# Optimization experiments

Hardware: AMD Instinct MI355X
Metric: run time of the kernel (lower is better)

## Reference

```python
import jax, jax.numpy as jnp
import numpy as np

NLAT, NLON = 64, 64
CIN = 512
HEADS = 8


def _cc_weights(n):
    # Clenshaw-Curtis quadrature weights on [-1, 1] for nodes cos(k*pi/(n-1)),
    # as used by torch-harmonics for the 'equiangular' grid. Weights sum to 2.
    N = n - 1
    theta = np.pi * np.arange(n) / N
    m = N // 2
    j = np.arange(1, m + 1)
    b = np.where(2 * j == N, 1.0, 2.0)
    S = (b / (4.0 * j ** 2 - 1.0))[None, :] * np.cos(2.0 * j[None, :] * theta[:, None])
    w = 1.0 - S.sum(axis=1)
    c = np.full(n, 2.0)
    c[0] = 1.0
    c[-1] = 1.0
    return c * w / N


def _log_quad_weights(nlat, nlon):
    # _precompute_latitudes flips nodes/weights; then 2*pi*w/nlon tiled over lon.
    w = _cc_weights(nlat)[::-1].copy()
    qw = 2.0 * np.pi * w / nlon                       # (nlat,)
    qw = np.tile(qw[:, None], (1, nlon)).reshape(-1)  # (nlat*nlon,)
    return jnp.asarray(np.log(qw), dtype=jnp.float32)


def setup_inputs() -> dict:
    key = jax.random.key(0)
    ks = jax.random.split(key, 5)
    s_qkv = float(np.sqrt(3.0 / CIN))   # scale for q/k/v 1x1-conv weights
    s_proj = float(np.sqrt(3.0 / CIN))  # out_channels == CIN
    u = lambda k, sh, s: jax.random.uniform(k, sh, jnp.float32, -s, s)
    return dict(
        query=jax.random.normal(ks[0], (1, CIN, NLAT, NLON), jnp.float32),
        q_w=u(ks[1], (CIN, CIN), s_qkv), q_b=jnp.zeros((CIN,), jnp.float32),
        k_w=u(ks[2], (CIN, CIN), s_qkv), k_b=jnp.zeros((CIN,), jnp.float32),
        v_w=u(ks[3], (CIN, CIN), s_qkv), v_b=jnp.zeros((CIN,), jnp.float32),
        p_w=u(ks[4], (CIN, CIN), s_proj), p_b=jnp.zeros((CIN,), jnp.float32),
        log_quad_weights=_log_quad_weights(NLAT, NLON),
    )


def reference(query, q_w, q_b, k_w, k_b, v_w, v_b, p_w, p_b, log_quad_weights):
    B, C, H, W = query.shape
    hd = C // HEADS  # head dim (k_channels == out_channels == in_channels)

    def proj_tokens(x, w, b):
        # 1x1 conv == channel matmul, then split heads and flatten H*W tokens
        y = jnp.einsum('bihw,oi->bohw', x, w) + b[None, :, None, None]
        return y.reshape(B, HEADS, -1, H, W).transpose(0, 1, 3, 4, 2).reshape(B, HEADS, H * W, -1)

    q = proj_tokens(query, q_w, q_b)  # (B, heads, HW, hd)
    k = proj_tokens(query, k_w, k_b)  # self-attention: key/value default to query
    v = proj_tokens(query, v_w, v_b)

    scale = 1.0 / jnp.sqrt(jnp.asarray(hd, dtype=q.dtype))
    # additive log-quadrature bias over keys (broadcast over batch/head/query)
    logits = jnp.einsum('bhqd,bhkd->bhqk', q, k) * scale + log_quad_weights[None, None, None, :]
    attn = jax.nn.softmax(logits, axis=-1)
    out = jnp.einsum('bhqk,bhkd->bhqd', attn, v)          # (B, heads, HW, hd)
    out = out.transpose(0, 1, 3, 2).reshape(B, HEADS * hd, H, W)
    return jnp.einsum('bihw,oi->bohw', out, p_w) + p_b[None, :, None, None]
```

## Files before the change

### kernel.cpp

```cpp
#include <hip/hip_runtime.h>

typedef unsigned short u16;
typedef unsigned int u32;
typedef __bf16 bf16x8 __attribute__((ext_vector_type(8)));
typedef float f32x4 __attribute__((ext_vector_type(4)));
typedef unsigned short u16x4 __attribute__((ext_vector_type(4)));

#define LOG2E 1.4426950408889634f

#if __has_builtin(__builtin_amdgcn_exp2f)
#define EXP2F(x) __builtin_amdgcn_exp2f(x)
#else
#define EXP2F(x) exp2f(x)
#endif

__device__ __forceinline__ u16 f2bf(float f) {
    union { float f; u32 u; } a; a.f = f;
    u32 u = a.u;
    u += 0x7FFFu + ((u >> 16) & 1u);
    return (u16)(u >> 16);
}
__device__ __forceinline__ bf16x8 ldg8(const u16* p) {
    return *reinterpret_cast<const bf16x8*>(p);
}
#if __has_builtin(__builtin_amdgcn_cvt_pk_bf16_f32)
__device__ __forceinline__ u32 pack2(float a, float b) {
    auto r = __builtin_amdgcn_cvt_pk_bf16_f32(a, b);
    return __builtin_bit_cast(u32, r);
}
#else
__device__ __forceinline__ u32 pack2(float a, float b) {
    u32 ua = __float_as_uint(a) + 0x8000u;
    u32 ub = __float_as_uint(b) + 0x8000u;
    return __builtin_amdgcn_perm(ub, ua, 0x07060302);
}
#endif
__device__ __forceinline__ void async16(const void* g, void* l) {
    __builtin_amdgcn_global_load_lds(
        (const __attribute__((address_space(1))) u32*)g,
        (__attribute__((address_space(3))) u32*)l, 16, 0, 0);
}

#define MFMA16(a, b, c) __builtin_amdgcn_mfma_f32_16x16x32_bf16((a), (b), (c), 0, 0, 0)

__global__ __launch_bounds__(256) void prep(const float* __restrict__ X,
                                            u16* __restrict__ Xt,
                                            const float* __restrict__ s0,
                                            const float* __restrict__ s1,
                                            const float* __restrict__ s2,
                                            const float* __restrict__ s3,
                                            u16* __restrict__ Wqkv,
                                            u16* __restrict__ Wp,
                                            const float* __restrict__ lqw,
                                            float* __restrict__ lqw2g) {
    __shared__ u16 tile[64][65];
    const int tid = threadIdx.x;
    const int y = blockIdx.y;

    if (y < 8) {
        const int t0 = blockIdx.x * 64;
        const int c0 = y * 64;
#pragma unroll
        for (int i = 0; i < 16; ++i) {
            int idx = tid + i * 256;
            int r = idx >> 6, cc = idx & 63;
            tile[r][cc] = f2bf(X[(size_t)(c0 + r) * 4096 + t0 + cc]);
        }
        __syncthreads();
#pragma unroll
        for (int i = 0; i < 16; ++i) {
            int idx = tid + i * 256;
            int tr = idx >> 6, cc = idx & 63;
            Xt[(size_t)(t0 + tr) * 512 + c0 + cc] = tile[cc][tr];
        }
    } else if (y < 12) {
        const int m = y - 8;
        const float* s = (m == 0) ? s0 : (m == 1) ? s1 : (m == 2) ? s2 : s3;
        u16* d = (m == 3) ? Wp : Wqkv + (size_t)m * 262144;
#pragma unroll
        for (int j = 0; j < 4; ++j) {
            int i = blockIdx.x * 1024 + j * 256 + tid;
            float4 v = reinterpret_cast<const float4*>(s)[i];
            u16x4 o;
            o[0] = f2bf(v.x); o[1] = f2bf(v.y); o[2] = f2bf(v.z); o[3] = f2bf(v.w);
            reinterpret_cast<u16x4*>(d)[i] = o;
        }
    } else {
        if (blockIdx.x < 4) {
            int i = blockIdx.x * 256 + tid;
            float4 v = reinterpret_cast<const float4*>(lqw)[i];
            v.x *= LOG2E; v.y *= LOG2E; v.z *= LOG2E; v.w *= LOG2E;
            reinterpret_cast<float4*>(lqw2g)[i] = v;
        }
    }
}

__global__ __launch_bounds__(512, 2) void qkv_gemm(const u16* __restrict__ Wqkv,
                                                   const u16* __restrict__ Xt,
                                                   const float* __restrict__ qb,
                                                   const float* __restrict__ kb,
                                                   const float* __restrict__ vb,
                                                   u16* __restrict__ Qt,
                                                   u16* __restrict__ Kt,
                                                   u16* __restrict__ Vimg) {
    __shared__ __align__(16) u16 Al[2][128 * 32];
    __shared__ __align__(16) u16 Bl[2][128 * 32];

    const int tid = threadIdx.x;
    const int w = tid >> 6, lane = tid & 63;
    const int quad = lane >> 4, lm = lane & 15;
    const int wm = w & 1, wn = w >> 1;
    const int n0 = blockIdx.x * 128;
    const int my = blockIdx.y;
    const int m0 = my * 128;

    const int arow = lane >> 2;
    const int sch = (lane & 3) ^ ((lane >> 3) & 3);
    const u16* agp = Wqkv + (size_t)(m0 + w * 16 + arow) * 512 + sch * 8;
    const u16* bgp = Xt + (size_t)(n0 + w * 16 + arow) * 512 + sch * 8;

    async16(agp, &Al[0][w * 16 * 32]);
    async16(bgp, &Bl[0][w * 16 * 32]);
    agp += 32; bgp += 32;

    const int FOFF = lm * 64 + ((quad ^ ((lm >> 1) & 3)) << 4);

    f32x4 acc[4][2];
#pragma unroll
    for (int mt = 0; mt < 4; ++mt)
#pragma unroll
        for (int bt = 0; bt < 2; ++bt) acc[mt][bt] = (f32x4){0.f, 0.f, 0.f, 0.f};

    __syncthreads();

    for (int s = 0; s < 16; ++s) {
        const int buf = s & 1;
        if (s < 15) {
            async16(agp, &Al[buf ^ 1][w * 16 * 32]);
            async16(bgp, &Bl[buf ^ 1][w * 16 * 32]);
            agp += 32; bgp += 32;
        }
        const char* Ab = (const char*)&Al[buf][0];
        const char* Bb = (const char*)&Bl[buf][0];
        bf16x8 af[4], bfr[2];
#pragma unroll
        for (int mt = 0; mt < 4; ++mt)
            af[mt] = *(const bf16x8*)(Ab + wm * 4096 + mt * 1024 + FOFF);
#pragma unroll
        for (int bt = 0; bt < 2; ++bt)
            bfr[bt] = *(const bf16x8*)(Bb + wn * 2048 + bt * 1024 + FOFF);
#pragma unroll
        for (int mt = 0; mt < 4; ++mt)
#pragma unroll
            for (int bt = 0; bt < 2; ++bt)
                acc[mt][bt] = MFMA16(af[mt], bfr[bt], acc[mt][bt]);
        __syncthreads();
    }

    const int mat = my >> 2;
    const float* bias = (mat == 0) ? qb : (mat == 1) ? kb : vb;
    const int chbase = (my & 3) * 128 + wm * 64 + quad * 4;

    if (mat < 2) {
        u16* out = mat ? Kt : Qt;
        const float sc = mat ? 1.0f : 0.125f * LOG2E;
#pragma unroll
        for (int mt = 0; mt < 4; ++mt) {
            const int ch = chbase + mt * 16;
            float4 bv = *(const float4*)(bias + ch);
            float bvf[4] = {bv.x, bv.y, bv.z, bv.w};
#pragma unroll
            for (int bt = 0; bt < 2; ++bt) {
                int tok = n0 + wn * 32 + bt * 16 + lm;
                u16x4 pk;
#pragma unroll
                for (int r = 0; r < 4; ++r)
                    pk[r] = f2bf((acc[mt][bt][r] + bvf[r]) * sc);
                *(u16x4*)(out + (size_t)tok * 512 + ch) = pk;
            }
        }
    } else {
#pragma unroll
        for (int mt = 0; mt < 4; ++mt) {
            const int ch = chbase + mt * 16;
            float4 bv = *(const float4*)(bias + ch);
            float bvf[4] = {bv.x, bv.y, bv.z, bv.w};
            const int hh = ch >> 6;
            const int D0 = ch & 63;
#pragma unroll
            for (int bt = 0; bt < 2; ++bt) {
                int g = bt * 16 + lm;
                int key2 = 8 * ((g >> 2) & 3) + 4 * ((g >> 4) & 1) + (g & 3);
                int t = (n0 >> 5) + wn;
                int kc = key2 >> 3, ke = key2 & 7;
                u16* vdst = Vimg + (size_t)(hh * 128 + t) * 2048 + ke;
#pragma unroll
                for (int r = 0; r < 4; ++r) {
                    int D = D0 + r;
                    int lane_i = kc * 16 + ((D >> 1) & 7) * 2 + (D & 1);
                    vdst[(size_t)(D >> 4) * 512 + lane_i * 8] = f2bf(acc[mt][bt][r] + bvf[r]);
                }
            }
        }
    }
}

__global__ __launch_bounds__(256, 2) void out_gemm(const u16* __restrict__ Wp,
                                                   const u16* __restrict__ Ot,
                                                   const float* __restrict__ pb,
                                                   float* __restrict__ out) {
    __shared__ __align__(16) u16 Al[2][128 * 32];
    __shared__ __align__(16) u16 Bl[2][64 * 32];

    const int tid = threadIdx.x;
    const int w = tid >> 6, lane = tid & 63;
    const int quad = lane >> 4, lm = lane & 15;
    const int wm = w & 1, wn = w >> 1;
    const int n0 = blockIdx.x * 64;
    const int m0 = blockIdx.y * 128;

    const int arow = lane >> 2;
    const int sch = (lane & 3) ^ ((lane >> 3) & 3);
    const u16* agp0 = Wp + (size_t)(m0 + w * 16 + arow) * 512 + sch * 8;
    const u16* agp1 = agp0 + (size_t)64 * 512;
    const u16* bgp = Ot + (size_t)(n0 + w * 16 + arow) * 512 + sch * 8;

    async16(agp0, &Al[0][w * 16 * 32]);
    async16(agp1, &Al[0][(64 + w * 16) * 32]);
    async16(bgp, &Bl[0][w * 16 * 32]);
    agp0 += 32; agp1 += 32; bgp += 32;

    const int FOFF = lm * 64 + ((quad ^ ((lm >> 1) & 3)) << 4);

    f32x4 acc[4][2];
#pragma unroll
    for (int mt = 0; mt < 4; ++mt)
#pragma unroll
        for (int bt = 0; bt < 2; ++bt) acc[mt][bt] = (f32x4){0.f, 0.f, 0.f, 0.f};

    __syncthreads();

    for (int s = 0; s < 16; ++s) {
        const int buf = s & 1;
        if (s < 15) {
            async16(agp0, &Al[buf ^ 1][w * 16 * 32]);
            async16(agp1, &Al[buf ^ 1][(64 + w * 16) * 32]);
            async16(bgp, &Bl[buf ^ 1][w * 16 * 32]);
            agp0 += 32; agp1 += 32; bgp += 32;
        }
        const char* Ab = (const char*)&Al[buf][0];
        const char* Bb = (const char*)&Bl[buf][0];
        bf16x8 af[4], bfr[2];
#pragma unroll
        for (int mt = 0; mt < 4; ++mt)
            af[mt] = *(const bf16x8*)(Ab + wm * 4096 + mt * 1024 + FOFF);
#pragma unroll
        for (int bt = 0; bt < 2; ++bt)
            bfr[bt] = *(const bf16x8*)(Bb + wn * 2048 + bt * 1024 + FOFF);
#pragma unroll
        for (int mt = 0; mt < 4; ++mt)
#pragma unroll
            for (int bt = 0; bt < 2; ++bt)
                acc[mt][bt] = MFMA16(af[mt], bfr[bt], acc[mt][bt]);
        __syncthreads();
    }

#pragma unroll
    for (int mt = 0; mt < 4; ++mt) {
        const int ch = m0 + wm * 64 + mt * 16 + quad * 4;
        float4 bv = *(const float4*)(pb + ch);
        float bvf[4] = {bv.x, bv.y, bv.z, bv.w};
#pragma unroll
        for (int bt = 0; bt < 2; ++bt) {
            int tok = n0 + wn * 32 + bt * 16 + lm;
#pragma unroll
            for (int r = 0; r < 4; ++r)
                out[(size_t)(ch + r) * 4096 + tok] = acc[mt][bt][r] + bvf[r];
        }
    }
}

#define WAITVM(N) asm volatile("s_waitcnt vmcnt(" #N ")" ::: "memory")

__global__ __launch_bounds__(256, 2) void flash_attn(const u16* __restrict__ Qt,
                                                     const u16* __restrict__ Kt,
                                                     const u16* __restrict__ Vimg,
                                                     const float* __restrict__ lqw2g,
                                                     u16* __restrict__ Ot) {
    __shared__ __align__(16) char smem[65536];

    const int tid = threadIdx.x;
    const int w = tid >> 6, lane = tid & 63;
    const int quad = lane >> 4, lm = lane & 15;
    const int bid = blockIdx.x;
    const int h = bid & 7, hq = h * 64;
    const int q0 = (bid >> 3) * 64;
    const int kstart = w * 1024;

    char* kvw = smem + w * 8192;

    const int srow = lane >> 3;
    const int schunk = (lane & 7) ^ srow;
    const u16* kg = Kt + (size_t)(kstart + srow) * 512 + hq + schunk * 8;

    const u16* vp = Vimg + (size_t)(h * 128 + w * 32) * 2048 + (size_t)lane * 8;

    bf16x8 bq0[4], bq1[4];
#pragma unroll
    for (int s = 0; s < 4; ++s) {
        const u16* qb = Qt + (size_t)(q0 + s * 16 + lm) * 512 + hq + quad * 8;
        bq0[s] = ldg8(qb);
        bq1[s] = ldg8(qb + 32);
    }

    f32x4 breg0 = *(const f32x4*)(lqw2g + kstart + quad * 4);
    f32x4 breg1 = *(const f32x4*)(lqw2g + kstart + 16 + quad * 4);
    const float* bptr = lqw2g + kstart + 32 + quad * 4;

    const int A0 = lm * 128 + ((quad ^ (lm & 7)) << 4);
    const int A1 = A0 ^ 64;

#define STAGEK(DST)                                                            \
    {                                                                          \
        char* nb = (DST);                                                      \
        async16(kg, nb);                                                       \
        async16(kg + 8 * 512, nb + 1024);                                      \
        async16(kg + 16 * 512, nb + 2048);                                     \
        async16(kg + 24 * 512, nb + 3072);                                     \
        kg += 32 * 512;                                                        \
    }

    STAGEK(kvw)
    STAGEK(kvw + 4096)

    union { u32 u[4]; bf16x8 v; } onesu;
    onesu.u[0] = onesu.u[1] = onesu.u[2] = onesu.u[3] = 0x3F803F80u;
    const bf16x8 onesv = onesu.v;

    f32x4 acc_o[4][4];
#pragma unroll
    for (int mt = 0; mt < 4; ++mt)
#pragma unroll
        for (int s = 0; s < 4; ++s) acc_o[mt][s] = (f32x4){0.f, 0.f, 0.f, 0.f};
    f32x4 acc_l[4];
#pragma unroll
    for (int s = 0; s < 4; ++s) acc_l[s] = (f32x4){0.f, 0.f, 0.f, 0.f};

    union { u32 u[4]; bf16x8 v; } pb_[4];
    bf16x8 pv0, pv1, pv2, pv3;
    int bufsel = 0;

#define BODY(WN, DOBIAS, DOSTAGE, DOPV)                                        \
    {                                                                          \
        WAITVM(WN);                                                            \
        bf16x8 nv0 = ldg8(vp);                                                 \
        bf16x8 nv1 = ldg8(vp + 512);                                           \
        bf16x8 nv2 = ldg8(vp + 1024);                                          \
        bf16x8 nv3 = ldg8(vp + 1536);                                          \
        vp += 2048;                                                            \
        const char* Kb = kvw + bufsel;                                         \
        bf16x8 k00 = *(const bf16x8*)(Kb + A0);                                \
        bf16x8 k01 = *(const bf16x8*)(Kb + A1);                                \
        bf16x8 k10 = *(const bf16x8*)(Kb + 2048 + A0);                         \
        bf16x8 k11 = *(const bf16x8*)(Kb + 2048 + A1);                         \
        if (DOPV) {                                                            \
            _Pragma("unroll")                                                  \
            for (int s = 0; s < 4; ++s) {                                      \
                acc_o[0][s] = MFMA16(pv0, pb_[s].v, acc_o[0][s]);              \
                acc_o[1][s] = MFMA16(pv1, pb_[s].v, acc_o[1][s]);              \
                acc_o[2][s] = MFMA16(pv2, pb_[s].v, acc_o[2][s]);              \
                acc_o[3][s] = MFMA16(pv3, pb_[s].v, acc_o[3][s]);              \
                acc_l[s] = MFMA16(onesv, pb_[s].v, acc_l[s]);                  \
            }                                                                  \
        }                                                                      \
        _Pragma("unroll")                                                      \
        for (int s = 0; s < 4; ++s) {                                          \
            f32x4 a = MFMA16(k00, bq0[s], breg0);                              \
            a = MFMA16(k01, bq1[s], a);                                        \
            pb_[s].u[0] = pack2(EXP2F(a[0]), EXP2F(a[1]));                     \
            pb_[s].u[1] = pack2(EXP2F(a[2]), EXP2F(a[3]));                     \
        }                                                                      \
        _Pragma("unroll")                                                      \
        for (int s = 0; s < 4; ++s) {                                          \
            f32x4 c = MFMA16(k10, bq0[s], breg1);                              \
            c = MFMA16(k11, bq1[s], c);                                        \
            pb_[s].u[2] = pack2(EXP2F(c[0]), EXP2F(c[1]));                     \
            pb_[s].u[3] = pack2(EXP2F(c[2]), EXP2F(c[3]));                     \
        }                                                                      \
        if (DOBIAS) {                                                          \
            breg0 = *(const f32x4*)(bptr);                                     \
            breg1 = *(const f32x4*)(bptr + 16);                                \
            bptr += 32;                                                        \
        }                                                                      \
        pv0 = nv0; pv1 = nv1; pv2 = nv2; pv3 = nv3;                            \
        if (DOSTAGE) STAGEK(kvw + bufsel)                                      \
        bufsel ^= 4096;                                                        \
    }

    BODY(4, true, true, false)
    for (int t = 1; t < 30; ++t)
        BODY(10, true, true, true)
    BODY(6, true, false, true)
    BODY(2, false, false, true)

#undef BODY
#undef STAGEK

#pragma unroll
    for (int s = 0; s < 4; ++s) {
        acc_o[0][s] = MFMA16(pv0, pb_[s].v, acc_o[0][s]);
        acc_o[1][s] = MFMA16(pv1, pb_[s].v, acc_o[1][s]);
        acc_o[2][s] = MFMA16(pv2, pb_[s].v, acc_o[2][s]);
        acc_o[3][s] = MFMA16(pv3, pb_[s].v, acc_o[3][s]);
        acc_l[s] = MFMA16(onesv, pb_[s].v, acc_l[s]);
    }

    __syncthreads();
    float* mbuf = (float*)smem;
    if (w != 0) {
        float* ob = mbuf + (w - 1) * 4096;
#pragma unroll
        for (int s = 0; s < 4; ++s) {
            const int r = s * 16 + lm;
#pragma unroll
            for (int mt = 0; mt < 4; ++mt) {
                const int sl = (mt * 4 + quad) ^ lm;
                *(f32x4*)(ob + r * 64 + sl * 4) = acc_o[mt][s];
            }
        }
        if (quad == 0) {
#pragma unroll
            for (int s = 0; s < 4; ++s)
                mbuf[12288 + (w - 1) * 64 + s * 16 + lm] = acc_l[s][0];
        }
    }
    __syncthreads();
    if (w != 0) return;

#pragma unroll
    for (int s = 0; s < 4; ++s) {
        const int r = s * 16 + lm;
        float lsum = acc_l[s][0];
#pragma unroll
        for (int p = 0; p < 3; ++p)
            lsum += mbuf[12288 + p * 64 + r];
        const float inv = 1.0f / lsum;
#pragma unroll
        for (int mt = 0; mt < 4; ++mt) {
            const int sl = (mt * 4 + quad) ^ lm;
            f32x4 o = acc_o[mt][s];
#pragma unroll
            for (int p = 0; p < 3; ++p)
                o += *(const f32x4*)(mbuf + p * 4096 + r * 64 + sl * 4);
            u16x4 pkv;
#pragma unroll
            for (int r2 = 0; r2 < 4; ++r2)
                pkv[r2] = f2bf(o[r2] * inv);
            *reinterpret_cast<u16x4*>(Ot + (size_t)(q0 + r) * 512 +
                                      hq + mt * 16 + quad * 4) = pkv;
        }
    }
}

extern "C" void kernel_launch(void* const* d_in, const int* in_sizes, int n_in,
                              void* d_out, int out_size, void* d_ws, size_t ws_size,
                              hipStream_t stream) {
    (void)in_sizes; (void)n_in; (void)out_size; (void)ws_size;
    const float* X   = (const float*)d_in[0];
    const float* qw  = (const float*)d_in[1];
    const float* qb  = (const float*)d_in[2];
    const float* kw  = (const float*)d_in[3];
    const float* kb  = (const float*)d_in[4];
    const float* vw  = (const float*)d_in[5];
    const float* vb  = (const float*)d_in[6];
    const float* pw  = (const float*)d_in[7];
    const float* pb  = (const float*)d_in[8];
    const float* lqw = (const float*)d_in[9];

    const size_t E = (size_t)4096 * 512;
    const size_t WE = (size_t)512 * 512;
    u16* Xt    = (u16*)d_ws;
    u16* Qt    = Xt + E;
    u16* Kt    = Qt + E;
    u16* Vimg  = Kt + E;
    u16* Wqkv  = Vimg + E;
    u16* Wp    = Wqkv + 3 * WE;
    float* lqw2g = (float*)(Wp + WE);
    u16* Ot    = Xt;

    prep<<<dim3(64, 13), dim3(256), 0, stream>>>(X, Xt, qw, kw, vw, pw,
                                                 Wqkv, Wp, lqw, lqw2g);
    qkv_gemm<<<dim3(32, 12), dim3(512), 0, stream>>>(Wqkv, Xt, qb, kb, vb, Qt, Kt, Vimg);
    flash_attn<<<dim3(512), dim3(256), 0, stream>>>(Qt, Kt, Vimg, lqw2g, Ot);
    out_gemm<<<dim3(64, 4), dim3(256), 0, stream>>>(Wp, Ot, pb, (float*)d_out);
}
```

Measured before the change: 77.39 us.

## Store K in MFMA fragment layout and load directly to registers in attention

The QKV GEMM now writes K in a pre-swizzled fragment image, like V, so the attention kernel can load K fragments straight from global memory into registers with double buffering instead of staging through LDS with async copies and vmcnt waits. The row-sum is now accumulated with scalar adds of the exponentials instead of an extra MFMA against a ones vector, and it is reduced across waves through a small LDS buffer. This removes LDS traffic and the ones-MFMA, and shrinks shared memory, which could allow higher occupancy. In exchange it relies on register-resident prefetch to hide global latency and adds VALU adds per tile.

```diff
diff --git a/kernel.cpp b/kernel.cpp
--- a/kernel.cpp
+++ b/kernel.cpp
@@ -101,7 +101,7 @@
                                                    const float* __restrict__ kb,
                                                    const float* __restrict__ vb,
                                                    u16* __restrict__ Qt,
-                                                   u16* __restrict__ Kt,
+                                                   u16* __restrict__ Kimg,
                                                    u16* __restrict__ Vimg) {
     __shared__ __align__(16) u16 Al[2][128 * 32];
     __shared__ __align__(16) u16 Bl[2][128 * 32];
@@ -161,9 +161,8 @@
     const float* bias = (mat == 0) ? qb : (mat == 1) ? kb : vb;
     const int chbase = (my & 3) * 128 + wm * 64 + quad * 4;
 
-    if (mat < 2) {
-        u16* out = mat ? Kt : Qt;
-        const float sc = mat ? 1.0f : 0.125f * LOG2E;
+    if (mat == 0) {
+        const float sc = 0.125f * LOG2E;
 #pragma unroll
         for (int mt = 0; mt < 4; ++mt) {
             const int ch = chbase + mt * 16;
@@ -176,7 +175,31 @@
 #pragma unroll
                 for (int r = 0; r < 4; ++r)
                     pk[r] = f2bf((acc[mt][bt][r] + bvf[r]) * sc);
-                *(u16x4*)(out + (size_t)tok * 512 + ch) = pk;
+                *(u16x4*)(Qt + (size_t)tok * 512 + ch) = pk;
+            }
+        }
+    } else if (mat == 1) {
+#pragma unroll
+        for (int mt = 0; mt < 4; ++mt) {
+            const int ch = chbase + mt * 16;
+            float4 bv = *(const float4*)(bias + ch);
+            float bvf[4] = {bv.x, bv.y, bv.z, bv.w};
+            const int hh = ch >> 6;
+            const int D0 = ch & 63;
+            const int cq = (D0 >> 3) & 3;
+            const int dh = D0 >> 5;
+            const int e0 = D0 & 7;
+#pragma unroll
+            for (int bt = 0; bt < 2; ++bt) {
+                int tok = n0 + wn * 32 + bt * 16 + lm;
+                int t = tok >> 5;
+                int kh = (tok >> 4) & 1;
+                u16x4 pk;
+#pragma unroll
+                for (int r = 0; r < 4; ++r)
+                    pk[r] = f2bf(acc[mt][bt][r] + bvf[r]);
+                *(u16x4*)(Kimg + (size_t)(hh * 128 + t) * 2048 +
+                          (kh * 2 + dh) * 512 + (cq * 16 + lm) * 8 + e0) = pk;
             }
         }
     } else {
@@ -280,14 +303,12 @@
     }
 }
 
-#define WAITVM(N) asm volatile("s_waitcnt vmcnt(" #N ")" ::: "memory")
-
 __global__ __launch_bounds__(256, 2) void flash_attn(const u16* __restrict__ Qt,
-                                                     const u16* __restrict__ Kt,
+                                                     const u16* __restrict__ Kimg,
                                                      const u16* __restrict__ Vimg,
                                                      const float* __restrict__ lqw2g,
                                                      u16* __restrict__ Ot) {
-    __shared__ __align__(16) char smem[65536];
+    __shared__ __align__(16) float smem[13600];
 
     const int tid = threadIdx.x;
     const int w = tid >> 6, lane = tid & 63;
@@ -297,12 +318,7 @@
     const int q0 = (bid >> 3) * 64;
     const int kstart = w * 1024;
 
-    char* kvw = smem + w * 8192;
-
-    const int srow = lane >> 3;
-    const int schunk = (lane & 7) ^ srow;
-    const u16* kg = Kt + (size_t)(kstart + srow) * 512 + hq + schunk * 8;
-
+    const u16* kp = Kimg + (size_t)(h * 128 + w * 32) * 2048 + (size_t)lane * 8;
     const u16* vp = Vimg + (size_t)(h * 128 + w * 32) * 2048 + (size_t)lane * 8;
 
     bf16x8 bq0[4], bq1[4];
@@ -317,106 +333,91 @@
     f32x4 breg1 = *(const f32x4*)(lqw2g + kstart + 16 + quad * 4);
     const float* bptr = lqw2g + kstart + 32 + quad * 4;
 
-    const int A0 = lm * 128 + ((quad ^ (lm & 7)) << 4);
-    const int A1 = A0 ^ 64;
-
-#define STAGEK(DST)                                                            \
+    f32x4 acc_o[4][4];
+#pragma unroll
+    for (int mt = 0; mt < 4; ++mt)
+#pragma unroll
+        for (int s = 0; s < 4; ++s) acc_o[mt][s] = (f32x4){0.f, 0.f, 0.f, 0.f};
+    float psum[4] = {0.f, 0.f, 0.f, 0.f};
+
+    bf16x8 kA0, kA1, kA2, kA3, kB0, kB1, kB2, kB3;
+    bf16x8 vA0, vA1, vA2, vA3, vB0, vB1, vB2, vB3;
+    union { u32 u[4]; bf16x8 v; } pb_[4];
+
+    kA0 = ldg8(kp); kA1 = ldg8(kp + 512); kA2 = ldg8(kp + 1024); kA3 = ldg8(kp + 1536);
+    kp += 2048;
+
+#define BODY(KC0, KC1, KC2, KC3, KN0, KN1, KN2, KN3,                           \
+             VC0, VC1, VC2, VC3, VN0, VN1, VN2, VN3, DOLDK, DOBIAS, DOPV)      \
     {                                                                          \
-        char* nb = (DST);                                                      \
-        async16(kg, nb);                                                       \
-        async16(kg + 8 * 512, nb + 1024);                                      \
-        async16(kg + 16 * 512, nb + 2048);                                     \
-        async16(kg + 24 * 512, nb + 3072);                                     \
-        kg += 32 * 512;                                                        \
-    }
-
-    STAGEK(kvw)
-    STAGEK(kvw + 4096)
-
-    union { u32 u[4]; bf16x8 v; } onesu;
-    onesu.u[0] = onesu.u[1] = onesu.u[2] = onesu.u[3] = 0x3F803F80u;
-    const bf16x8 onesv = onesu.v;
-
-    f32x4 acc_o[4][4];
-#pragma unroll
-    for (int mt = 0; mt < 4; ++mt)
-#pragma unroll
-        for (int s = 0; s < 4; ++s) acc_o[mt][s] = (f32x4){0.f, 0.f, 0.f, 0.f};
-    f32x4 acc_l[4];
-#pragma unroll
-    for (int s = 0; s < 4; ++s) acc_l[s] = (f32x4){0.f, 0.f, 0.f, 0.f};
-
-    union { u32 u[4]; bf16x8 v; } pb_[4];
-    bf16x8 pv0, pv1, pv2, pv3;
-    int bufsel = 0;
-
-#define BODY(WN, DOBIAS, DOSTAGE, DOPV)                                        \
-    {                                                                          \
-        WAITVM(WN);                                                            \
-        bf16x8 nv0 = ldg8(vp);                                                 \
-        bf16x8 nv1 = ldg8(vp + 512);                                           \
-        bf16x8 nv2 = ldg8(vp + 1024);                                          \
-        bf16x8 nv3 = ldg8(vp + 1536);                                          \
+        VN0 = ldg8(vp); VN1 = ldg8(vp + 512);                                  \
+        VN2 = ldg8(vp + 1024); VN3 = ldg8(vp + 1536);                          \
         vp += 2048;                                                            \
-        const char* Kb = kvw + bufsel;                                         \
-        bf16x8 k00 = *(const bf16x8*)(Kb + A0);                                \
-        bf16x8 k01 = *(const bf16x8*)(Kb + A1);                                \
-        bf16x8 k10 = *(const bf16x8*)(Kb + 2048 + A0);                         \
-        bf16x8 k11 = *(const bf16x8*)(Kb + 2048 + A1);                         \
+        if (DOLDK) {                                                           \
+            KN0 = ldg8(kp); KN1 = ldg8(kp + 512);                              \
+            KN2 = ldg8(kp + 1024); KN3 = ldg8(kp + 1536);                      \
+            kp += 2048;                                                        \
+        }                                                                      \
         if (DOPV) {                                                            \
             _Pragma("unroll")                                                  \
             for (int s = 0; s < 4; ++s) {                                      \
-                acc_o[0][s] = MFMA16(pv0, pb_[s].v, acc_o[0][s]);              \
-                acc_o[1][s] = MFMA16(pv1, pb_[s].v, acc_o[1][s]);              \
-                acc_o[2][s] = MFMA16(pv2, pb_[s].v, acc_o[2][s]);              \
-                acc_o[3][s] = MFMA16(pv3, pb_[s].v, acc_o[3][s]);              \
-                acc_l[s] = MFMA16(onesv, pb_[s].v, acc_l[s]);                  \
+                acc_o[0][s] = MFMA16(VC0, pb_[s].v, acc_o[0][s]);              \
+                acc_o[1][s] = MFMA16(VC1, pb_[s].v, acc_o[1][s]);              \
+                acc_o[2][s] = MFMA16(VC2, pb_[s].v, acc_o[2][s]);              \
+                acc_o[3][s] = MFMA16(VC3, pb_[s].v, acc_o[3][s]);              \
             }                                                                  \
         }                                                                      \
         _Pragma("unroll")                                                      \
         for (int s = 0; s < 4; ++s) {                                          \
-            f32x4 a = MFMA16(k00, bq0[s], breg0);                              \
-            a = MFMA16(k01, bq1[s], a);                                        \
-            pb_[s].u[0] = pack2(EXP2F(a[0]), EXP2F(a[1]));                     \
-            pb_[s].u[1] = pack2(EXP2F(a[2]), EXP2F(a[3]));                     \
-        }                                                                      \
-        _Pragma("unroll")                                                      \
-        for (int s = 0; s < 4; ++s) {                                          \
-            f32x4 c = MFMA16(k10, bq0[s], breg1);                              \
-            c = MFMA16(k11, bq1[s], c);                                        \
-            pb_[s].u[2] = pack2(EXP2F(c[0]), EXP2F(c[1]));                     \
-            pb_[s].u[3] = pack2(EXP2F(c[2]), EXP2F(c[3]));                     \
+            f32x4 a = MFMA16(KC0, bq0[s], breg0);                              \
+            a = MFMA16(KC1, bq1[s], a);                                        \
+            float e0 = EXP2F(a[0]), e1 = EXP2F(a[1]);                          \
+            float e2 = EXP2F(a[2]), e3 = EXP2F(a[3]);                          \
+            psum[s] += (e0 + e1) + (e2 + e3);                                  \
+            pb_[s].u[0] = pack2(e0, e1);                                       \
+            pb_[s].u[1] = pack2(e2, e3);                                       \
+            f32x4 c = MFMA16(KC2, bq0[s], breg1);                              \
+            c = MFMA16(KC3, bq1[s], c);                                        \
+            float f0 = EXP2F(c[0]), f1 = EXP2F(c[1]);                          \
+            float f2 = EXP2F(c[2]), f3 = EXP2F(c[3]);                          \
+            psum[s] += (f0 + f1) + (f2 + f3);                                  \
+            pb_[s].u[2] = pack2(f0, f1);                                       \
+            pb_[s].u[3] = pack2(f2, f3);                                       \
         }                                                                      \
         if (DOBIAS) {                                                          \
             breg0 = *(const f32x4*)(bptr);                                     \
             breg1 = *(const f32x4*)(bptr + 16);                                \
             bptr += 32;                                                        \
         }                                                                      \
-        pv0 = nv0; pv1 = nv1; pv2 = nv2; pv3 = nv3;                            \
-        if (DOSTAGE) STAGEK(kvw + bufsel)                                      \
-        bufsel ^= 4096;                                                        \
-    }
-
-    BODY(4, true, true, false)
-    for (int t = 1; t < 30; ++t)
-        BODY(10, true, true, true)
-    BODY(6, true, false, true)
-    BODY(2, false, false, true)
-
+    }
+
+    BODY(kA0, kA1, kA2, kA3, kB0, kB1, kB2, kB3,
+         vB0, vB1, vB2, vB3, vA0, vA1, vA2, vA3, true, true, false)
+    for (int i = 0; i < 15; ++i) {
+        BODY(kB0, kB1, kB2, kB3, kA0, kA1, kA2, kA3,
+             vA0, vA1, vA2, vA3, vB0, vB1, vB2, vB3, true, true, true)
+        BODY(kA0, kA1, kA2, kA3, kB0, kB1, kB2, kB3,
+             vB0, vB1, vB2, vB3, vA0, vA1, vA2, vA3, true, true, true)
+    }
+    BODY(kB0, kB1, kB2, kB3, kA0, kA1, kA2, kA3,
+         vA0, vA1, vA2, vA3, vB0, vB1, vB2, vB3, false, false, true)
 #undef BODY
-#undef STAGEK
 
 #pragma unroll
     for (int s = 0; s < 4; ++s) {
-        acc_o[0][s] = MFMA16(pv0, pb_[s].v, acc_o[0][s]);
-        acc_o[1][s] = MFMA16(pv1, pb_[s].v, acc_o[1][s]);
-        acc_o[2][s] = MFMA16(pv2, pb_[s].v, acc_o[2][s]);
-        acc_o[3][s] = MFMA16(pv3, pb_[s].v, acc_o[3][s]);
-        acc_l[s] = MFMA16(onesv, pb_[s].v, acc_l[s]);
-    }
-
-    __syncthreads();
-    float* mbuf = (float*)smem;
+        acc_o[0][s] = MFMA16(vB0, pb_[s].v, acc_o[0][s]);
+        acc_o[1][s] = MFMA16(vB1, pb_[s].v, acc_o[1][s]);
+        acc_o[2][s] = MFMA16(vB2, pb_[s].v, acc_o[2][s]);
+        acc_o[3][s] = MFMA16(vB3, pb_[s].v, acc_o[3][s]);
+    }
+
+    float* mbuf = smem;
+    float* lbuf = smem + 12288;
+
+#pragma unroll
+    for (int s = 0; s < 4; ++s)
+        lbuf[(s * 16 + lm) * 20 + w * 4 + quad] = psum[s];
+
     if (w != 0) {
         float* ob = mbuf + (w - 1) * 4096;
 #pragma unroll
@@ -428,11 +429,6 @@
                 *(f32x4*)(ob + r * 64 + sl * 4) = acc_o[mt][s];
             }
         }
-        if (quad == 0) {
-#pragma unroll
-            for (int s = 0; s < 4; ++s)
-                mbuf[12288 + (w - 1) * 64 + s * 16 + lm] = acc_l[s][0];
-        }
     }
     __syncthreads();
     if (w != 0) return;
@@ -440,11 +436,11 @@
 #pragma unroll
     for (int s = 0; s < 4; ++s) {
         const int r = s * 16 + lm;
-        float lsum = acc_l[s][0];
-#pragma unroll
-        for (int p = 0; p < 3; ++p)
-            lsum += mbuf[12288 + p * 64 + r];
-        const float inv = 1.0f / lsum;
+        f32x4 lv = (f32x4){0.f, 0.f, 0.f, 0.f};
+#pragma unroll
+        for (int j = 0; j < 4; ++j)
+            lv += *(const f32x4*)(lbuf + r * 20 + j * 4);
+        const float inv = 1.0f / ((lv[0] + lv[1]) + (lv[2] + lv[3]));
 #pragma unroll
         for (int mt = 0; mt < 4; ++mt) {
             const int sl = (mt * 4 + quad) ^ lm;
@@ -481,8 +477,8 @@
     const size_t WE = (size_t)512 * 512;
     u16* Xt    = (u16*)d_ws;
     u16* Qt    = Xt + E;
-    u16* Kt    = Qt + E;
-    u16* Vimg  = Kt + E;
+    u16* Kimg  = Qt + E;
+    u16* Vimg  = Kimg + E;
     u16* Wqkv  = Vimg + E;
     u16* Wp    = Wqkv + 3 * WE;
     float* lqw2g = (float*)(Wp + WE);
@@ -490,7 +486,7 @@
 
     prep<<<dim3(64, 13), dim3(256), 0, stream>>>(X, Xt, qw, kw, vw, pw,
                                                  Wqkv, Wp, lqw, lqw2g);
-    qkv_gemm<<<dim3(32, 12), dim3(512), 0, stream>>>(Wqkv, Xt, qb, kb, vb, Qt, Kt, Vimg);
-    flash_attn<<<dim3(512), dim3(256), 0, stream>>>(Qt, Kt, Vimg, lqw2g, Ot);
+    qkv_gemm<<<dim3(32, 12), dim3(512), 0, stream>>>(Wqkv, Xt, qb, kb, vb, Qt, Kimg, Vimg);
+    flash_attn<<<dim3(512), dim3(256), 0, stream>>>(Qt, Kimg, Vimg, lqw2g, Ot);
     out_gemm<<<dim3(64, 4), dim3(256), 0, stream>>>(Wp, Ot, pb, (float*)d_out);
 }
```

Result: no change. 77.49 us (+0.1%).
